# Performance work log

Measured on AMD Instinct MI355X. Metric: run time of the kernel, lower is better.

The kernel has to match this reference:

```python
import jax, jax.numpy as jnp
import numpy as np
import math

B, S, D, H, K = 8, 4096, 1024, 16, 256
DK = D // H


def setup_inputs() -> dict:
    key = jax.random.key(0)
    ks = jax.random.split(key, 8)
    s = 1.0 / math.sqrt(D)
    x = jax.random.normal(ks[0], (B, S, D), dtype=jnp.float32)
    Wq = jax.random.normal(ks[1], (D, D), dtype=jnp.float32) * s
    Wk = jax.random.normal(ks[2], (D, D), dtype=jnp.float32) * s
    Wv = jax.random.normal(ks[3], (D, D), dtype=jnp.float32) * s
    Wo = jax.random.normal(ks[4], (D, D), dtype=jnp.float32) * s
    bq = jnp.zeros((D,), jnp.float32)
    bk = jnp.zeros((D,), jnp.float32)
    bv = jnp.zeros((D,), jnp.float32)
    bo = jnp.zeros((D,), jnp.float32)
    # xavier-uniform-style scale for the low-rank projections
    lim = math.sqrt(6.0 / (S + K))
    E = jax.random.uniform(ks[5], (S, K), jnp.float32, -lim, lim)
    Fp = jax.random.uniform(ks[6], (S, K), jnp.float32, -lim, lim)
    return {"x": x, "Wq": Wq, "bq": bq, "Wk": Wk, "bk": bk,
            "Wv": Wv, "bv": bv, "Wo": Wo, "bo": bo, "E": E, "Fp": Fp}


def reference(x, Wq, bq, Wk, bk, Wv, bv, Wo, bo, E, Fp):
    b, s, d = x.shape
    # QKV projections, split heads: [b, h, s, dk]
    def heads(y):
        return y.reshape(b, s, H, DK).transpose(0, 2, 1, 3)
    Q = heads(x @ Wq + bq)
    Kh = heads(x @ Wk + bk)
    Vh = heads(x @ Wv + bv)
    # Low-rank projection of K, V along sequence: [b, h, k, dk]
    Kp = jnp.einsum('sk,bhsd->bhkd', E, Kh)
    Vp = jnp.einsum('sk,bhsd->bhkd', Fp, Vh)
    # Attention over projected length k
    scores = jnp.einsum('bhsd,bhkd->bhsk', Q, Kp) / math.sqrt(DK)
    attn = jax.nn.softmax(scores, axis=-1)
    out = jnp.einsum('bhsk,bhkd->bhsd', attn, Vp)
    out = out.transpose(0, 2, 1, 3).reshape(b, s, d)
    return out @ Wo + bo
```

## Files before the change

### kernel.cpp

```cpp
#include <hip/hip_runtime.h>

#define AS1 __attribute__((address_space(1)))
#define AS3 __attribute__((address_space(3)))

typedef __attribute__((ext_vector_type(8))) short s16x8;
typedef __attribute__((ext_vector_type(4))) float f32x4;
typedef __attribute__((ext_vector_type(4))) unsigned short u16x4;
typedef __attribute__((ext_vector_type(8))) unsigned short u16x8;

#define MFMA16(a, b, c) __builtin_amdgcn_mfma_f32_16x16x32_bf16(a, b, c, 0, 0, 0)

static __device__ __forceinline__ unsigned short f2bf(float f) {
  unsigned u = __builtin_bit_cast(unsigned, f);
  u += 0x7fffu + ((u >> 16) & 1u);
  return (unsigned short)(u >> 16);
}

static __device__ __forceinline__ void gll16(const unsigned short* g, char* l) {
  __builtin_amdgcn_global_load_lds((const AS1 void*)g, (AS3 void*)l, 16, 0, 0);
}

#define BAR() asm volatile("s_barrier" ::: "memory")
#define WAITV(N) asm volatile("s_waitcnt vmcnt(" #N ")" ::: "memory")
#define FENCE() asm volatile("" ::: "memory")

__device__ __forceinline__ void gemm256_pipe(const unsigned short* __restrict__ A0, int lda,
                                             const unsigned short* __restrict__ B0, int ldb,
                                             int NT2, char* lds, f32x4 (&acc)[8][4]) {
  const int t = threadIdx.x;
  const int lane = t & 63, w = t >> 6, g = lane >> 4, l15 = lane & 15;
  const int wm = w >> 2, wn = w & 3;
  char* const A_lds[2] = {lds, lds + 65536};
  char* const B_lds[2] = {lds + 32768, lds + 98304};
  s16x8 af[2][4], bfr[2][4];

  const int rl = t >> 3, sl = t & 7;
  const unsigned short* aB = A0 + (size_t)rl * lda + ((sl ^ (rl & 7)) << 3);
  const unsigned short* bB = B0 + (size_t)rl * ldb + ((sl ^ (rl & 7)) << 3);
  const int woff = w << 10;

  char* pA[2][2];
  char* pB[2][2];
#pragma unroll
  for (int b = 0; b < 2; ++b)
#pragma unroll
    for (int kk = 0; kk < 2; ++kk) {
      pA[b][kk] = lds + b * 65536 + (wm * 64 + l15) * 128 + (((kk * 4 + g) ^ (l15 & 7)) << 4);
      pB[b][kk] = lds + 32768 + b * 65536 + (wn * 32 + l15) * 128 + (((kk * 4 + g) ^ (l15 & 7)) << 4);
    }

#define STGA(BUF, H, PTR)                                                                \
  do {                                                                                   \
    gll16((PTR) + (size_t)((H)*128) * lda, A_lds[BUF] + woff + (H)*16384);               \
    gll16((PTR) + (size_t)((H)*128 + 64) * lda, A_lds[BUF] + woff + (H)*16384 + 8192);   \
  } while (0)
#define STGB(BUF, H, PTR)                                                                \
  do {                                                                                   \
    gll16((PTR) + (size_t)((H)*128) * ldb, B_lds[BUF] + woff + (H)*16384);               \
    gll16((PTR) + (size_t)((H)*128 + 64) * ldb, B_lds[BUF] + woff + (H)*16384 + 8192);   \
  } while (0)

#define LDAQ(BUF, QH)                                                                    \
  do {                                                                                   \
    _Pragma("unroll") for (int mi = 0; mi < 4; ++mi)                                     \
        _Pragma("unroll") for (int kk = 0; kk < 2; ++kk)                                 \
            af[kk][mi] = *(const s16x8*)(pA[BUF][kk] + (QH)*16384 + mi * 2048);          \
  } while (0)
#define LDBP(BUF, NH)                                                                    \
  do {                                                                                   \
    _Pragma("unroll") for (int ni = 0; ni < 2; ++ni)                                     \
        _Pragma("unroll") for (int kk = 0; kk < 2; ++kk)                                 \
            bfr[kk][(NH)*2 + ni] =                                                       \
                *(const s16x8*)(pB[BUF][kk] + (NH)*16384 + ni * 2048);                   \
  } while (0)
#define MQUAD(QH, NH)                                                                    \
  do {                                                                                   \
    __builtin_amdgcn_s_setprio(1);                                                       \
    _Pragma("unroll") for (int kk = 0; kk < 2; ++kk)                                     \
        _Pragma("unroll") for (int mi = 0; mi < 4; ++mi)                                 \
            _Pragma("unroll") for (int ni = 0; ni < 2; ++ni)                             \
                acc[(QH)*4 + mi][(NH)*2 + ni] =                                          \
        MFMA16(af[kk][mi], bfr[kk][(NH)*2 + ni], acc[(QH)*4 + mi][(NH)*2 + ni]);         \
    __builtin_amdgcn_s_setprio(0);                                                       \
  } while (0)

  STGA(0, 0, aB);
  STGB(0, 0, bB);
  STGB(0, 1, bB);
  STGA(0, 1, aB);
  STGA(1, 0, aB + 64);
  STGB(1, 0, bB + 64);
  STGB(1, 1, bB + 64);
  STGA(1, 1, aB + 64);
  WAITV(8);
  BAR();

  for (int it = 0; it < NT2; ++it) {
    const bool pf = (it + 1 < NT2);
    const unsigned short* aN = aB + it * 128 + 128;
    const unsigned short* bN = bB + it * 128 + 128;
    LDAQ(0, 0);
    LDBP(0, 0);
    MQUAD(0, 0);
    BAR();
    LDBP(0, 1);
    if (pf) { STGA(0, 0, aN); STGB(0, 0, bN); }
    MQUAD(0, 1);
    BAR();
    LDAQ(0, 1);
    if (pf) STGB(0, 1, bN);
    MQUAD(1, 0);
    BAR();
    if (pf) STGA(0, 1, aN);
    MQUAD(1, 1);
    if (pf) WAITV(8);
    else WAITV(0);
    BAR();
    LDAQ(1, 0);
    LDBP(1, 0);
    MQUAD(0, 0);
    BAR();
    LDBP(1, 1);
    if (pf) { STGA(1, 0, aN + 64); STGB(1, 0, bN + 64); }
    MQUAD(0, 1);
    BAR();
    LDAQ(1, 1);
    if (pf) STGB(1, 1, bN + 64);
    MQUAD(1, 0);
    BAR();
    if (pf) STGA(1, 1, aN + 64);
    MQUAD(1, 1);
    if (pf) WAITV(8);
    BAR();
  }
#undef STGA
#undef STGB
#undef LDAQ
#undef LDBP
#undef MQUAD
}

__global__ __launch_bounds__(512, 2) void k_gemm_q(const unsigned short* __restrict__ xb,
                                                   const unsigned short* __restrict__ Wqt,
                                                   const float* __restrict__ biasq,
                                                   unsigned short* __restrict__ Qb) {
  __shared__ __align__(16) char lds[131072];
  f32x4 acc[8][4];
#pragma unroll
  for (int i = 0; i < 8; ++i)
#pragma unroll
    for (int j = 0; j < 4; ++j) acc[i][j] = f32x4{0.f, 0.f, 0.f, 0.f};
  int bid = blockIdx.y * 4 + blockIdx.x;
  bid = (bid & 7) * 64 + (bid >> 3);
  const int bn = bid & 3, bm = bid >> 2;
  gemm256_pipe(xb + (size_t)bm * 256 * 1024, 1024, Wqt + (size_t)bn * 256 * 1024, 1024, 8, lds, acc);

  const int t = threadIdx.x, lane = t & 63, w = t >> 6, g = lane >> 4, l15 = lane & 15;
  const int wm = w >> 2, wn = w & 3;
  const float QSC = 0.1803368801111204f;
#pragma unroll
  for (int nf = 0; nf < 4; ++nf) {
    const int n = bn * 256 + (nf >> 1) * 128 + wn * 32 + (nf & 1) * 16 + l15;
    const float bias = biasq[n];
#pragma unroll
    for (int mq = 0; mq < 8; ++mq) {
      const int m0 = bm * 256 + (mq >> 2) * 128 + wm * 64 + (mq & 3) * 16 + g * 4;
      const f32x4 v = acc[mq][nf];
#pragma unroll
      for (int r = 0; r < 4; ++r) Qb[(size_t)(m0 + r) * 1024 + n] = f2bf((v[r] + bias) * QSC);
    }
  }
}

__global__ __launch_bounds__(512, 2) void k_gemm_out(const unsigned short* __restrict__ AO,
                                                     const unsigned short* __restrict__ Wot,
                                                     const float* __restrict__ bo,
                                                     float* __restrict__ out) {
  __shared__ __align__(16) char lds[131072];
  f32x4 acc[8][4];
#pragma unroll
  for (int i = 0; i < 8; ++i)
#pragma unroll
    for (int j = 0; j < 4; ++j) acc[i][j] = f32x4{0.f, 0.f, 0.f, 0.f};
  int bid = blockIdx.y * 4 + blockIdx.x;
  bid = (bid & 7) * 64 + (bid >> 3);
  const int bn = bid & 3, bm = bid >> 2;
  gemm256_pipe(AO + (size_t)bm * 256 * 1024, 1024, Wot + (size_t)bn * 256 * 1024, 1024, 8, lds, acc);

  const int t = threadIdx.x, lane = t & 63, w = t >> 6, g = lane >> 4, l15 = lane & 15;
  const int wm = w >> 2, wn = w & 3;
#pragma unroll
  for (int nf = 0; nf < 4; ++nf) {
    const int n = bn * 256 + (nf >> 1) * 128 + wn * 32 + (nf & 1) * 16 + l15;
    const float bias = bo[n];
#pragma unroll
    for (int mq = 0; mq < 8; ++mq) {
      const int m0 = bm * 256 + (mq >> 2) * 128 + wm * 64 + (mq & 3) * 16 + g * 4;
      const f32x4 v = acc[mq][nf];
#pragma unroll
      for (int r = 0; r < 4; ++r) out[(size_t)(m0 + r) * 1024 + n] = v[r] + bias;
    }
  }
}

__device__ __forceinline__ void gemm_tile(const unsigned short* __restrict__ Ab, int lda,
                                          const unsigned short* __restrict__ Bb, int ldb,
                                          int Kc, char* lds, f32x4 (&acc)[4][4]) {
  const int t = threadIdx.x;
  const int lane = t & 63, w = t >> 6, g = lane >> 4, l15 = lane & 15;
  const int wm = w >> 1, wn = w & 1;
  char* As = lds;
  char* Bs = lds + 16384;
  for (int ks = 0; ks < Kc; ks += 64) {
    __syncthreads();
#pragma unroll
    for (int i = 0; i < 4; ++i) {
      const int c = i * 256 + t, row = c >> 3, sl = c & 7;
      const int col = ks + ((sl ^ (row & 7)) << 3);
      const int ubase = (i * 256 + w * 64) << 4;
      gll16(Ab + (size_t)row * lda + col, As + ubase);
      gll16(Bb + (size_t)row * ldb + col, Bs + ubase);
    }
    __syncthreads();
    s16x8 af[2][4], bfr[2][4];
#pragma unroll
    for (int kk = 0; kk < 2; ++kk)
#pragma unroll
      for (int x4 = 0; x4 < 4; ++x4) {
        const int ra = wm * 64 + x4 * 16 + l15;
        const int rb = wn * 64 + x4 * 16 + l15;
        af[kk][x4] = *(const s16x8*)(As + ra * 128 + ((((kk << 2) + g) ^ (ra & 7)) << 4));
        bfr[kk][x4] = *(const s16x8*)(Bs + rb * 128 + ((((kk << 2) + g) ^ (rb & 7)) << 4));
      }
#pragma unroll
    for (int kk = 0; kk < 2; ++kk)
#pragma unroll
      for (int mt = 0; mt < 4; ++mt)
#pragma unroll
        for (int nt = 0; nt < 4; ++nt)
          acc[mt][nt] = MFMA16(af[kk][mt], bfr[kk][nt], acc[mt][nt]);
  }
}

__global__ __launch_bounds__(256) void k_gemm_xef(const unsigned short* __restrict__ Et,
                                                  const unsigned short* __restrict__ Ft,
                                                  const unsigned short* __restrict__ xbT,
                                                  unsigned short* __restrict__ xEF) {
  __shared__ __align__(16) char lds[32768];
  f32x4 acc[4][4];
#pragma unroll
  for (int i = 0; i < 4; ++i)
#pragma unroll
    for (int j = 0; j < 4; ++j) acc[i][j] = f32x4{0.f, 0.f, 0.f, 0.f};
  const int b = blockIdx.z >> 1, ef = blockIdx.z & 1;
  const unsigned short* Ab = (ef ? Ft : Et) + blockIdx.y * 128 * 4096;
  const unsigned short* Bb = xbT + (size_t)b * 4194304 + blockIdx.x * 128 * 4096;
  gemm_tile(Ab, 4096, Bb, 4096, 4096, lds, acc);

  const int t = threadIdx.x, lane = t & 63, w = t >> 6, g = lane >> 4, l15 = lane & 15;
  const int wm = w >> 1, wn = w & 1;
  const int nb = blockIdx.x * 128 + wn * 64, mb = blockIdx.y * 128 + wm * 64;
  unsigned short* C = xEF + (size_t)(b * 2 + ef) * 262144;
#pragma unroll
  for (int nt = 0; nt < 4; ++nt) {
    const int n = nb + nt * 16 + l15;
#pragma unroll
    for (int mt = 0; mt < 4; ++mt) {
      const int m0 = mb + mt * 16 + g * 4;
      const f32x4 v = acc[mt][nt];
#pragma unroll
      for (int r = 0; r < 4; ++r) C[(m0 + r) * 1024 + n] = f2bf(v[r]);
    }
  }
}

__global__ __launch_bounds__(256) void k_kpvp2(const unsigned short* __restrict__ xEF,
                                               const unsigned short* __restrict__ Wqkvt,
                                               const float* __restrict__ biasq,
                                               const float* __restrict__ sEF,
                                               unsigned short* __restrict__ Kp,
                                               unsigned short* __restrict__ VpT) {
  __shared__ __align__(16) char lds[32768];
  f32x4 acc[4][4];
#pragma unroll
  for (int i = 0; i < 4; ++i)
#pragma unroll
    for (int j = 0; j < 4; ++j) acc[i][j] = f32x4{0.f, 0.f, 0.f, 0.f};
  const int b = blockIdx.z >> 1, kv = blockIdx.z & 1;
  const unsigned short* Ab = xEF + (size_t)(b * 2 + kv) * 262144 + blockIdx.y * 128 * 1024;
  const unsigned short* Bb = Wqkvt + (size_t)(1 + kv) * 1048576 + blockIdx.x * 128 * 1024;
  gemm_tile(Ab, 1024, Bb, 1024, 1024, lds, acc);

  const int t = threadIdx.x, lane = t & 63, w = t >> 6, g = lane >> 4, l15 = lane & 15;
  const int wm = w >> 1, wn = w & 1;
  const int nb = blockIdx.x * 128 + wn * 64, mb = blockIdx.y * 128 + wm * 64;
  const float* bias = biasq + (1 + kv) * 1024;
  const float* sE = sEF + kv * 256;
  if (!kv) {
    unsigned short* C = Kp + b * 262144;
#pragma unroll
    for (int nt = 0; nt < 4; ++nt) {
      const int n = nb + nt * 16 + l15;
      const float bn_ = bias[n];
#pragma unroll
      for (int mt = 0; mt < 4; ++mt) {
        const int m0 = mb + mt * 16 + g * 4;
        const f32x4 v = acc[mt][nt];
#pragma unroll
        for (int r = 0; r < 4; ++r) C[(m0 + r) * 1024 + n] = f2bf(v[r] + sE[m0 + r] * bn_);
      }
    }
  } else {
    unsigned short* C = VpT + b * 262144;
#pragma unroll
    for (int nt = 0; nt < 4; ++nt) {
      const int n = nb + nt * 16 + l15;
      const float bn_ = bias[n];
#pragma unroll
      for (int mt = 0; mt < 4; ++mt) {
        const int m0 = mb + mt * 16 + g * 4;
        const f32x4 v = acc[mt][nt];
        u16x4 pk;
#pragma unroll
        for (int r = 0; r < 4; ++r) pk[r] = f2bf(v[r] + sE[m0 + r] * bn_);
        *(u16x4*)(C + (n << 8) + m0) = pk;
      }
    }
  }
}

__global__ __launch_bounds__(512, 2) void k_attn(const unsigned short* __restrict__ Qb,
                                                 const unsigned short* __restrict__ Kp,
                                                 const unsigned short* __restrict__ VpT,
                                                 unsigned short* __restrict__ AO) {
  __shared__ __align__(16) char lds[131072];
  char* K0 = lds;
  char* V0 = lds + 32768;
  char* Qd = lds + 65536;
  char* Pb = lds + 98304;
  const int t = threadIdx.x, lane = t & 63, w = t >> 6, g = lane >> 4, l15 = lane & 15;
  const int sh = blockIdx.x, h = blockIdx.y, b = blockIdx.z;
  const int s0 = sh * 2048;
  const unsigned short* Qg = Qb + (size_t)(b * 4096 + s0) * 1024 + h * 64;
  const unsigned short* Kg = Kp + b * 262144 + h * 64;
  const unsigned short* Vg = VpT + b * 262144 + (h * 64) * 256;

#pragma unroll
  for (int i = 0; i < 4; ++i) {
    const int c = i * 512 + t, row = c >> 3, slr = c & 7;
    gll16(Kg + row * 1024 + ((slr ^ (row & 7)) << 3), K0 + ((i * 512 + w * 64) << 4));
  }
#pragma unroll
  for (int i = 0; i < 4; ++i) {
    const int c = i * 512 + t, row = c >> 5, slr = c & 31;
    gll16(Vg + row * 256 + ((slr ^ (row & 7)) << 3), V0 + ((i * 512 + w * 64) << 4));
  }
#pragma unroll
  for (int i = 0; i < 2; ++i) {
    const int c = i * 512 + t, row = c >> 3, slr = c & 7;
    gll16(Qg + row * 1024 + ((slr ^ (row & 7)) << 3), Qd + ((i * 512 + w * 64) << 4));
  }
  __syncthreads();

  char* const PwRow = Pb + (w << 12) + l15 * 256;
  const int wOffP = (g * 8 + l15 * 16) & 255;
  const int qrow = w * 16 + l15;
  const int qsw0 = (g ^ (qrow & 7)) << 4;
  const int qsw1 = ((4 + g) ^ (qrow & 7)) << 4;

  for (int st = 0; st < 16; ++st) {
    char* qb = Qd + ((st & 1) << 14);
    const s16x8 aq0 = *(const s16x8*)(qb + qrow * 128 + qsw0);
    const s16x8 aq1 = *(const s16x8*)(qb + qrow * 128 + qsw1);
    if (st < 15) {
      const unsigned short* Qn = Qg + (size_t)(st + 1) * 131072;
      char* qn = Qd + (((st + 1) & 1) << 14);
#pragma unroll
      for (int i = 0; i < 2; ++i) {
        const int c = i * 512 + t, row = c >> 3, slr = c & 7;
        gll16(Qn + row * 1024 + ((slr ^ (row & 7)) << 3), qn + ((i * 512 + w * 64) << 4));
      }
    }

    f32x4 sc[16];
#pragma unroll
    for (int nt = 0; nt < 16; ++nt) sc[nt] = f32x4{0.f, 0.f, 0.f, 0.f};
#pragma unroll
    for (int nt = 0; nt < 16; ++nt) {
      const int row = nt * 16 + l15;
      const s16x8 b0 = *(const s16x8*)(K0 + row * 128 + ((g ^ (row & 7)) << 4));
      const s16x8 b1 = *(const s16x8*)(K0 + row * 128 + (((4 + g) ^ (row & 7)) << 4));
      sc[nt] = MFMA16(b0, aq0, sc[nt]);
      sc[nt] = MFMA16(b1, aq1, sc[nt]);
    }

    float sm_ = 0.f;
    f32x4 ov[4];
#pragma unroll
    for (int nt = 0; nt < 4; ++nt) ov[nt] = f32x4{0.f, 0.f, 0.f, 0.f};

#pragma unroll
    for (int half = 0; half < 2; ++half) {
#pragma unroll
      for (int nt2 = 0; nt2 < 8; ++nt2) {
        const f32x4 s4 = sc[half * 8 + nt2];
        const float p0 = __builtin_amdgcn_exp2f(s4[0]);
        const float p1 = __builtin_amdgcn_exp2f(s4[1]);
        const float p2 = __builtin_amdgcn_exp2f(s4[2]);
        const float p3 = __builtin_amdgcn_exp2f(s4[3]);
        sm_ += (p0 + p1) + (p2 + p3);
        u16x4 pk;
        pk[0] = f2bf(p0);
        pk[1] = f2bf(p1);
        pk[2] = f2bf(p2);
        pk[3] = f2bf(p3);
        *(u16x4*)(PwRow + ((nt2 * 32 + wOffP) & 255)) = pk;
      }
      FENCE();
#pragma unroll
      for (int kk = 0; kk < 4; ++kk) {
        const int slh = ((kk * 4 + g + l15) & 15) << 4;
        const s16x8 ap = *(const s16x8*)(PwRow + slh);
#pragma unroll
        for (int nt = 0; nt < 4; ++nt) {
          const int rv = nt * 16 + l15;
          const int slot = half * 16 + (kk << 2) + g;
          const s16x8 bv = *(const s16x8*)(V0 + rv * 512 + ((slot ^ (rv & 7)) << 4));
          ov[nt] = MFMA16(ap, bv, ov[nt]);
        }
      }
      FENCE();
    }
    sm_ += __shfl_xor(sm_, 16);
    sm_ += __shfl_xor(sm_, 32);
    const float inv = 1.f / sm_;
    float invr[4];
#pragma unroll
    for (int r = 0; r < 4; ++r) invr[r] = __shfl(inv, (g << 2) + r);

    unsigned short* Ao = AO + (size_t)(b * 4096 + s0 + st * 128 + w * 16) * 1024 + h * 64;
#pragma unroll
    for (int nt = 0; nt < 4; ++nt) {
#pragma unroll
      for (int r = 0; r < 4; ++r) {
        Ao[(g * 4 + r) * 1024 + nt * 16 + l15] = f2bf(ov[nt][r] * invr[r]);
      }
    }
    __syncthreads();
  }
}

__global__ __launch_bounds__(256) void k_cvt_xt(const float* __restrict__ x,
                                                unsigned short* __restrict__ xb,
                                                unsigned short* __restrict__ xbT) {
  __shared__ unsigned short tl[64][66];
  const int t = threadIdx.x;
  const int rt = blockIdx.x >> 4, ct = blockIdx.x & 15;
  const int s0g = rt * 64, d0 = ct * 64;
  const int lr = t >> 4, lc4 = (t & 15) * 4;
#pragma unroll
  for (int p = 0; p < 4; ++p) {
    const int row = s0g + p * 16 + lr;
    const float4 v = *(const float4*)(x + (size_t)row * 1024 + d0 + lc4);
    u16x4 o;
    o[0] = f2bf(v.x);
    o[1] = f2bf(v.y);
    o[2] = f2bf(v.z);
    o[3] = f2bf(v.w);
    *(u16x4*)(xb + (size_t)row * 1024 + d0 + lc4) = o;
    const int tr = p * 16 + lr;
    tl[tr][lc4] = o[0];
    tl[tr][lc4 + 1] = o[1];
    tl[tr][lc4 + 2] = o[2];
    tl[tr][lc4 + 3] = o[3];
  }
  __syncthreads();
  const int dr = t >> 2, sc = (t & 3) * 16;
  u16x8 tmp[2];
  unsigned short* tp = (unsigned short*)tmp;
#pragma unroll
  for (int i = 0; i < 16; ++i) tp[i] = tl[sc + i][dr];
  const int b = s0g >> 12, slr = s0g & 4095;
  unsigned short* dst = xbT + (size_t)b * 4194304 + (size_t)(d0 + dr) * 4096 + slr + sc;
  *(u16x8*)(dst) = tmp[0];
  *(u16x8*)(dst + 8) = tmp[1];
}

__global__ __launch_bounds__(256) void k_colsum1(const float* __restrict__ E,
                                                 const float* __restrict__ Fp,
                                                 float* __restrict__ part) {
  const int sc = blockIdx.x, ef = blockIdx.y, k = threadIdx.x;
  const float* M = ef ? Fp : E;
  float s = 0.f;
#pragma unroll 4
  for (int i = 0; i < 256; ++i) s += M[(size_t)((sc << 8) + i) * 256 + k];
  part[(ef * 16 + sc) * 256 + k] = s;
}

__global__ __launch_bounds__(256) void k_prep(const float* __restrict__ Wq, const float* __restrict__ Wk,
                                              const float* __restrict__ Wv, const float* __restrict__ Wo,
                                              const float* __restrict__ E, const float* __restrict__ Fp,
                                              const float* __restrict__ bq, const float* __restrict__ bk,
                                              const float* __restrict__ bv,
                                              const float* __restrict__ part,
                                              unsigned short* __restrict__ Wqkvt, unsigned short* __restrict__ Wot,
                                              unsigned short* __restrict__ Et, unsigned short* __restrict__ Ft,
                                              float* __restrict__ biasq, float* __restrict__ sEF) {
  const int i = blockIdx.x * 256 + threadIdx.x;
  if (i < 3145728) {
    const int gsel = i >> 20, rem = i & 1048575, n = rem >> 10, k = rem & 1023;
    const float* W = gsel == 0 ? Wq : (gsel == 1 ? Wk : Wv);
    Wqkvt[i] = f2bf(W[(k << 10) + n]);
  } else if (i < 4194304) {
    const int j = i - 3145728, n = j >> 10, k = j & 1023;
    Wot[j] = f2bf(Wo[(k << 10) + n]);
  } else if (i < 5242880) {
    const int j = i - 4194304, kp = j >> 12, s = j & 4095;
    Et[j] = f2bf(E[(s << 8) + kp]);
  } else if (i < 6291456) {
    const int j = i - 5242880, kp = j >> 12, s = j & 4095;
    Ft[j] = f2bf(Fp[(s << 8) + kp]);
  } else if (i < 6294528) {
    const int j = i - 6291456;
    biasq[j] = (j < 1024) ? bq[j] : (j < 2048 ? bk[j - 1024] : bv[j - 2048]);
  } else if (i < 6295040) {
    const int j = i - 6294528;
    const int ef = j >> 8, k = j & 255;
    float s = 0.f;
#pragma unroll
    for (int c = 0; c < 16; ++c) s += part[(ef * 16 + c) * 256 + k];
    sEF[j] = s;
  }
}

extern "C" void kernel_launch(void* const* d_in, const int* in_sizes, int n_in,
                              void* d_out, int out_size, void* d_ws, size_t ws_size,
                              hipStream_t stream) {
  const float* x = (const float*)d_in[0];
  const float* Wq = (const float*)d_in[1];
  const float* bq = (const float*)d_in[2];
  const float* Wk = (const float*)d_in[3];
  const float* bk = (const float*)d_in[4];
  const float* Wv = (const float*)d_in[5];
  const float* bv = (const float*)d_in[6];
  const float* Wo = (const float*)d_in[7];
  const float* bo = (const float*)d_in[8];
  const float* E = (const float*)d_in[9];
  const float* Fp = (const float*)d_in[10];

  char* ws = (char*)d_ws;
  size_t off = 0;
  auto alloc = [&](size_t bytes) {
    char* p = ws + off;
    off += (bytes + 255) & ~(size_t)255;
    return p;
  };
  unsigned short* xb = (unsigned short*)alloc(33554432ull * 2);
  unsigned short* xbT = (unsigned short*)alloc(33554432ull * 2);
  unsigned short* Qb = (unsigned short*)alloc(33554432ull * 2);
  unsigned short* Wqkvt = (unsigned short*)alloc(3145728ull * 2);
  unsigned short* Wot = (unsigned short*)alloc(1048576ull * 2);
  unsigned short* Et = (unsigned short*)alloc(1048576ull * 2);
  unsigned short* Ft = (unsigned short*)alloc(1048576ull * 2);
  unsigned short* xEF = (unsigned short*)alloc(4194304ull * 2);
  unsigned short* Kp = (unsigned short*)alloc(2097152ull * 2);
  unsigned short* VpT = (unsigned short*)alloc(2097152ull * 2);
  float* biasq = (float*)alloc(3072 * 4);
  float* part = (float*)alloc(8192 * 4);
  float* sEF = (float*)alloc(512 * 4);
  (void)in_sizes; (void)n_in; (void)out_size; (void)ws_size;

  k_cvt_xt<<<8192, 256, 0, stream>>>(x, xb, xbT);
  k_colsum1<<<dim3(16, 2), 256, 0, stream>>>(E, Fp, part);
  k_prep<<<24590, 256, 0, stream>>>(Wq, Wk, Wv, Wo, E, Fp, bq, bk, bv, part,
                                    Wqkvt, Wot, Et, Ft, biasq, sEF);
  k_gemm_q<<<dim3(4, 128), 512, 0, stream>>>(xb, Wqkvt, biasq, Qb);
  k_gemm_xef<<<dim3(8, 2, 16), 256, 0, stream>>>(Et, Ft, xbT, xEF);
  k_kpvp2<<<dim3(8, 2, 16), 256, 0, stream>>>(xEF, Wqkvt, biasq, sEF, Kp, VpT);
  k_attn<<<dim3(2, 16, 8), 512, 0, stream>>>(Qb, Kp, VpT, xb);
  k_gemm_out<<<dim3(4, 128), 512, 0, stream>>>(xb, Wot, bo, (float*)d_out);
}
```

Measured before the change: 429.6 us.

## Split-K the x·E/F projection GEMM with a separate reduction kernel

The sequence-projection GEMM (K=4096) ran only 256 blocks, which underfills the GPU. It now splits K into four slices, giving 1024 blocks that each write fp32 partials to a new 64 MB workspace. A new reduction kernel sums the partials and converts them to bf16. This trades extra global traffic (writing and reading the partials) and one more launch for better occupancy.

Result: no change. 423.5 us (-1.4%).

```diff
diff --git a/kernel.cpp b/kernel.cpp
--- a/kernel.cpp
+++ b/kernel.cpp
@@ -245,22 +245,23 @@
 __global__ __launch_bounds__(256) void k_gemm_xef(const unsigned short* __restrict__ Et,
                                                   const unsigned short* __restrict__ Ft,
                                                   const unsigned short* __restrict__ xbT,
-                                                  unsigned short* __restrict__ xEF) {
+                                                  float* __restrict__ pxef) {
   __shared__ __align__(16) char lds[32768];
   f32x4 acc[4][4];
 #pragma unroll
   for (int i = 0; i < 4; ++i)
 #pragma unroll
     for (int j = 0; j < 4; ++j) acc[i][j] = f32x4{0.f, 0.f, 0.f, 0.f};
-  const int b = blockIdx.z >> 1, ef = blockIdx.z & 1;
-  const unsigned short* Ab = (ef ? Ft : Et) + blockIdx.y * 128 * 4096;
-  const unsigned short* Bb = xbT + (size_t)b * 4194304 + blockIdx.x * 128 * 4096;
-  gemm_tile(Ab, 4096, Bb, 4096, 4096, lds, acc);
+  const int z = blockIdx.z;
+  const int ks = z >> 4, pair = z & 15, b = pair >> 1, ef = pair & 1;
+  const unsigned short* Ab = (ef ? Ft : Et) + blockIdx.y * 128 * 4096 + ks * 1024;
+  const unsigned short* Bb = xbT + (size_t)b * 4194304 + blockIdx.x * 128 * 4096 + ks * 1024;
+  gemm_tile(Ab, 4096, Bb, 4096, 1024, lds, acc);
 
   const int t = threadIdx.x, lane = t & 63, w = t >> 6, g = lane >> 4, l15 = lane & 15;
   const int wm = w >> 1, wn = w & 1;
   const int nb = blockIdx.x * 128 + wn * 64, mb = blockIdx.y * 128 + wm * 64;
-  unsigned short* C = xEF + (size_t)(b * 2 + ef) * 262144;
+  float* C = pxef + (size_t)z * 262144;
 #pragma unroll
   for (int nt = 0; nt < 4; ++nt) {
     const int n = nb + nt * 16 + l15;
@@ -269,9 +270,25 @@
       const int m0 = mb + mt * 16 + g * 4;
       const f32x4 v = acc[mt][nt];
 #pragma unroll
-      for (int r = 0; r < 4; ++r) C[(m0 + r) * 1024 + n] = f2bf(v[r]);
-    }
-  }
+      for (int r = 0; r < 4; ++r) C[(m0 + r) * 1024 + n] = v[r];
+    }
+  }
+}
+
+__global__ __launch_bounds__(256) void k_xef_red(const float* __restrict__ pxef,
+                                                 unsigned short* __restrict__ xEF) {
+  const int j = (blockIdx.x * 256 + threadIdx.x) * 4;
+  f32x4 s = *(const f32x4*)(pxef + j);
+#pragma unroll
+  for (int ks = 1; ks < 4; ++ks) {
+    const f32x4 p = *(const f32x4*)(pxef + (size_t)ks * 4194304 + j);
+#pragma unroll
+    for (int r = 0; r < 4; ++r) s[r] += p[r];
+  }
+  u16x4 o;
+#pragma unroll
+  for (int r = 0; r < 4; ++r) o[r] = f2bf(s[r]);
+  *(u16x4*)(xEF + j) = o;
 }
 
 __global__ __launch_bounds__(256) void k_kpvp2(const unsigned short* __restrict__ xEF,
@@ -565,6 +582,7 @@
   unsigned short* xEF = (unsigned short*)alloc(4194304ull * 2);
   unsigned short* Kp = (unsigned short*)alloc(2097152ull * 2);
   unsigned short* VpT = (unsigned short*)alloc(2097152ull * 2);
+  float* pxef = (float*)alloc(16777216ull * 4);
   float* biasq = (float*)alloc(3072 * 4);
   float* part = (float*)alloc(8192 * 4);
   float* sEF = (float*)alloc(512 * 4);
@@ -575,7 +593,8 @@
   k_prep<<<24590, 256, 0, stream>>>(Wq, Wk, Wv, Wo, E, Fp, bq, bk, bv, part,
                                     Wqkvt, Wot, Et, Ft, biasq, sEF);
   k_gemm_q<<<dim3(4, 128), 512, 0, stream>>>(xb, Wqkvt, biasq, Qb);
-  k_gemm_xef<<<dim3(8, 2, 16), 256, 0, stream>>>(Et, Ft, xbT, xEF);
+  k_gemm_xef<<<dim3(8, 2, 64), 256, 0, stream>>>(Et, Ft, xbT, pxef);
+  k_xef_red<<<4096, 256, 0, stream>>>(pxef, xEF);
   k_kpvp2<<<dim3(8, 2, 16), 256, 0, stream>>>(xEF, Wqkvt, biasq, sEF, Kp, VpT);
   k_attn<<<dim3(2, 16, 8), 512, 0, stream>>>(Qb, Kp, VpT, xb);
   k_gemm_out<<<dim3(4, 128), 512, 0, stream>>>(xb, Wot, bo, (float*)d_out);
```
